# Kernel tuning notes

Measured on AMD Instinct MI355X. Metric: run time of the kernel, lower is better.

The kernel has to match this reference:

```python
import jax, jax.numpy as jnp
import numpy as np

N, E, D_IN, HID, HEADS = 50000, 800000, 128, 32, 8
NEG_SLOPE = 0.2


def gat_conv(x, src, dst, W_src, W_dst, a_src, a_dst, b, heads, ch, concat):
    n = x.shape[0]
    hs = (x @ W_src).reshape(n, heads, ch)  # source-side features [N,H,C]
    hd = (x @ W_dst).reshape(n, heads, ch)  # dest-side features   [N,H,C]
    alpha_s = jnp.einsum('nhc,hc->nh', hs, a_src)  # [N,H]
    alpha_d = jnp.einsum('nhc,hc->nh', hd, a_dst)  # [N,H]
    e = jax.nn.leaky_relu(alpha_s[src] + alpha_d[dst], NEG_SLOPE)  # [E,H]
    # segment softmax over edges grouped by destination node
    m = jax.ops.segment_max(e, dst, num_segments=n)
    m = jnp.where(jnp.isfinite(m), m, 0.0)
    e = jnp.exp(e - jax.lax.stop_gradient(m)[dst])
    denom = jax.ops.segment_sum(e, dst, num_segments=n)
    alpha = e / (denom[dst] + 1e-16)  # [E,H]
    # weighted scatter-aggregate of source features to destinations
    out = jax.ops.segment_sum(hs[src] * alpha[:, :, None], dst, num_segments=n)  # [N,H,C]
    out = out.reshape(n, heads * ch) if concat else out.mean(axis=1)
    return out + b


def setup_inputs() -> dict:
    key = jax.random.key(0)
    ks = jax.random.split(key, 12)
    glorot = lambda k, shape: jax.random.normal(k, shape, jnp.float32) * np.sqrt(2.0 / (shape[0] + shape[-1]))
    x = jax.random.normal(ks[0], (N, D_IN), jnp.float32)
    edge_index = jax.random.randint(ks[1], (2, E), 0, N, jnp.int64)
    return {
        'x': x,
        'edge_index': edge_index,
        'W1_src': glorot(ks[2], (D_IN, HEADS * HID)),
        'W1_dst': glorot(ks[3], (D_IN, HEADS * HID)),
        'a1_src': glorot(ks[4], (HEADS, HID)),
        'a1_dst': glorot(ks[5], (HEADS, HID)),
        'b1': jnp.zeros((HEADS * HID,), jnp.float32),
        'W2_src': glorot(ks[6], (HEADS * HID, HID)),
        'W2_dst': glorot(ks[7], (HEADS * HID, HID)),
        'a2_src': glorot(ks[8], (1, HID)),
        'a2_dst': glorot(ks[9], (1, HID)),
        'b2': jnp.zeros((HID,), jnp.float32),
    }


def reference(x, edge_index, W1_src, W1_dst, a1_src, a1_dst, b1,
              W2_src, W2_dst, a2_src, a2_dst, b2):
    src, dst = edge_index[0], edge_index[1]
    h = gat_conv(x, src, dst, W1_src, W1_dst, a1_src, a1_dst, b1, HEADS, HID, True)
    h = jax.nn.relu(h)
    out = gat_conv(h, src, dst, W2_src, W2_dst, a2_src, a2_dst, b2, 1, HID, True)
    return out
```

## Files before the change

### kernel.cpp

```cpp
#include <hip/hip_runtime.h>
#include <hip/hip_bf16.h>

#define NEG_SLOPE 0.2f

typedef unsigned int uint;
typedef unsigned short ushort;
typedef __attribute__((ext_vector_type(8))) short short8;
typedef __attribute__((ext_vector_type(4))) float floatx4;

static __device__ __forceinline__ ushort f2bf(float f) {
    uint u = __float_as_uint(f);
    uint r = (u + 0x7fffu + ((u >> 16) & 1u)) >> 16;
    return (ushort)r;
}
static __device__ __forceinline__ float bf2f(uint s) {
    return __uint_as_float(s << 16);
}

__global__ __launch_bounds__(256) void convert_x(
    const float* __restrict__ x, ushort* __restrict__ xb, int total4) {
    int i = blockIdx.x * blockDim.x + threadIdx.x;
    if (i >= total4) return;
    float4 v = ((const float4*)x)[i];
    uint2 pk;
    pk.x = (uint)f2bf(v.x) | ((uint)f2bf(v.y) << 16);
    pk.y = (uint)f2bf(v.z) | ((uint)f2bf(v.w) << 16);
    ((uint2*)xb)[i] = pk;
}

__global__ __launch_bounds__(256) void prep_weights(
    const float* __restrict__ W1_src, const float* __restrict__ W2_src,
    const float* __restrict__ W1_dst, const float* __restrict__ a1_dst,
    const float* __restrict__ W2_dst, const float* __restrict__ a2_dst,
    ushort* __restrict__ W1t, ushort* __restrict__ W2t,
    float* __restrict__ wc1, float* __restrict__ wc2) {
    int i = blockIdx.x * blockDim.x + threadIdx.x;
    if (i < 32768) {
        int nc = i & 255, k = i >> 8;
        W1t[nc * 128 + k] = f2bf(W1_src[k * 256 + nc]);
    } else if (i < 32768 + 8192) {
        int i2 = i - 32768;
        int c = i2 & 31, k = i2 >> 5;
        W2t[c * 256 + k] = f2bf(W2_src[k * 32 + c]);
    } else if (i < 32768 + 8192 + 1024) {
        int i3 = i - 32768 - 8192;
        int k = i3 >> 3, h = i3 & 7;
        float s = 0.f;
#pragma unroll
        for (int c = 0; c < 32; ++c)
            s += W1_dst[k * 256 + h * 32 + c] * a1_dst[h * 32 + c];
        wc1[i3] = s;
    } else if (i < 32768 + 8192 + 1024 + 256) {
        int k = i - 32768 - 8192 - 1024;
        float s = 0.f;
#pragma unroll
        for (int c = 0; c < 32; ++c)
            s += W2_dst[k * 32 + c] * a2_dst[c];
        wc2[k] = s;
    }
}

__global__ __launch_bounds__(256) void hist_kernel(
    const int* __restrict__ dst, int* __restrict__ deg, int E) {
    int e = blockIdx.x * blockDim.x + threadIdx.x;
    if (e < E) atomicAdd(&deg[dst[e]], 1);
}

__global__ __launch_bounds__(256) void scan_block(
    const int* __restrict__ deg, int* __restrict__ incl,
    int* __restrict__ bsum, int n) {
    __shared__ int sh[256];
    int tid = threadIdx.x;
    int i = blockIdx.x * 256 + tid;
    sh[tid] = (i < n) ? deg[i] : 0;
    __syncthreads();
    for (int off = 1; off < 256; off <<= 1) {
        int t = (tid >= off) ? sh[tid - off] : 0;
        __syncthreads();
        sh[tid] += t;
        __syncthreads();
    }
    if (i < n) incl[i] = sh[tid];
    if (tid == 255) bsum[blockIdx.x] = sh[255];
}

__global__ __launch_bounds__(256) void scan_top(
    const int* __restrict__ bsum, int* __restrict__ boff, int nb) {
    __shared__ int sh[256];
    int tid = threadIdx.x;
    sh[tid] = (tid < nb) ? bsum[tid] : 0;
    __syncthreads();
    for (int off = 1; off < 256; off <<= 1) {
        int t = (tid >= off) ? sh[tid - off] : 0;
        __syncthreads();
        sh[tid] += t;
        __syncthreads();
    }
    boff[tid] = sh[tid] - ((tid < nb) ? bsum[tid] : 0);
}

__global__ __launch_bounds__(256) void rs_kernel(
    const int* __restrict__ incl, const int* __restrict__ deg,
    const int* __restrict__ boff, int* __restrict__ rs,
    int* __restrict__ cursor, int n) {
    int i = blockIdx.x * blockDim.x + threadIdx.x;
    if (i >= n) return;
    int v = incl[i] - deg[i] + boff[i >> 8];
    rs[i] = v;
    cursor[i] = v;
}

__global__ __launch_bounds__(256) void fill_kernel(
    const int* __restrict__ src, const int* __restrict__ dst,
    int* __restrict__ cursor, int* __restrict__ csr_src, int E) {
    int e = blockIdx.x * blockDim.x + threadIdx.x;
    if (e >= E) return;
    int d = dst[e];
    int pos = atomicAdd(&cursor[d], 1);
    csr_src[pos] = src[e];
}

__global__ __launch_bounds__(256) void gemm1_mfma(
    const ushort* __restrict__ xb, const ushort* __restrict__ W1t,
    const float* __restrict__ a_src, const float* __restrict__ wc1,
    ushort* __restrict__ hs1b, float* __restrict__ as1,
    float* __restrict__ ad1, int n) {
    __shared__ ushort At[128 * 128];
    __shared__ ushort Out[128 * 128];
    int mblk = blockIdx.x >> 1, nhalf = blockIdx.x & 1;
    int m0 = mblk * 128;
    int tid = threadIdx.x;
#pragma unroll
    for (int i = 0; i < 8; ++i) {
        int id = tid + i * 256;
        int m = id >> 4, c = id & 15;
        int gm = m0 + m;
        uint4 v = {0, 0, 0, 0};
        if (gm < n) v = *(const uint4*)(xb + (size_t)gm * 128 + c * 8);
        *(uint4*)(At + m * 128 + ((c ^ (m & 15)) * 8)) = v;
    }
    __syncthreads();
    int wid = tid >> 6, lane = tid & 63;
    int q = lane >> 4, l16 = lane & 15;
    int wm = (wid >> 1) * 64;
    int wn = (wid & 1) * 64;
    int gn0 = nhalf * 128 + wn;
    floatx4 z = {0.f, 0.f, 0.f, 0.f};
    floatx4 acc[4][4];
#pragma unroll
    for (int mt = 0; mt < 4; ++mt)
#pragma unroll
        for (int nt = 0; nt < 4; ++nt) acc[mt][nt] = z;
#pragma unroll
    for (int s = 0; s < 4; ++s) {
        short8 af[4], bf[4];
#pragma unroll
        for (int mt = 0; mt < 4; ++mt) {
            int row = wm + mt * 16 + l16;
            int c = s * 4 + q;
            af[mt] = *(const short8*)(At + row * 128 + ((c ^ (row & 15)) * 8));
        }
#pragma unroll
        for (int nt = 0; nt < 4; ++nt) {
            int col = gn0 + nt * 16 + l16;
            bf[nt] = *(const short8*)(W1t + col * 128 + s * 32 + q * 8);
        }
#pragma unroll
        for (int mt = 0; mt < 4; ++mt)
#pragma unroll
            for (int nt = 0; nt < 4; ++nt)
                acc[mt][nt] = __builtin_amdgcn_mfma_f32_16x16x32_bf16(
                    af[mt], bf[nt], acc[mt][nt], 0, 0, 0);
    }
#pragma unroll
    for (int mt = 0; mt < 4; ++mt)
#pragma unroll
        for (int nt = 0; nt < 4; ++nt) {
            floatx4 a = acc[mt][nt];
            int colL = wn + nt * 16 + l16;
#pragma unroll
            for (int r = 0; r < 4; ++r) {
                int rowL = wm + mt * 16 + q * 4 + r;
                Out[rowL * 128 + colL] = f2bf(a[r]);
            }
        }
    __syncthreads();
#pragma unroll
    for (int i = 0; i < 8; ++i) {
        int id = tid + i * 256;
        int m = id >> 4, c8 = id & 15;
        int gm = m0 + m;
        if (gm < n) {
            uint4 v = *(uint4*)(Out + m * 128 + c8 * 8);
            *(uint4*)(hs1b + (size_t)gm * 256 + nhalf * 128 + c8 * 8) = v;
        }
    }
#pragma unroll
    for (int i = 0; i < 2; ++i) {
        int id = tid + i * 256;
        int m = id & 127, hl = id >> 7;
        int gm = m0 + m;
        if (gm < n) {
            int h = nhalf * 4 + hl;
            const ushort* row = Out + m * 128 + hl * 32;
            const float* av = a_src + h * 32;
            float s = 0.f;
#pragma unroll
            for (int c = 0; c < 32; ++c) s += bf2f(row[c]) * av[c];
            as1[(size_t)gm * 8 + h] = s;
        }
    }
    if (nhalf == 0) {
#pragma unroll
        for (int i = 0; i < 4; ++i) {
            int id = tid + i * 256;
            int m = id & 127, h = id >> 7;
            int gm = m0 + m;
            if (gm < n) {
                float s = 0.f;
                for (int c = 0; c < 16; ++c) {
                    const ushort* p = At + m * 128 + ((c ^ (m & 15)) * 8);
#pragma unroll
                    for (int jj = 0; jj < 8; ++jj)
                        s += bf2f(p[jj]) * wc1[(c * 8 + jj) * 8 + h];
                }
                ad1[(size_t)gm * 8 + h] = s;
            }
        }
    }
}

__global__ __launch_bounds__(256) void gather1(
    const int* __restrict__ csr_src, const int* __restrict__ rs,
    const int* __restrict__ deg, const ushort* __restrict__ hs1b,
    const float* __restrict__ as1, const float* __restrict__ ad1,
    const float* __restrict__ b1, ushort* __restrict__ h1b, int n) {
    int gid = blockIdx.x * blockDim.x + threadIdx.x;
    int node = gid >> 6;
    int lane = threadIdx.x & 63;
    if (node >= n) return;
    int j = lane >> 5, l = lane & 31;
    int h = l >> 2;
    float ad_v = ad1[node * 8 + h];
    int start = rs[node], cnt = deg[node];
    float acc0 = 0.f, acc1 = 0.f, acc2 = 0.f, acc3 = 0.f;
    float acc4 = 0.f, acc5 = 0.f, acc6 = 0.f, acc7 = 0.f;
    float dacc = 0.f;
    int i = j;
    for (; i + 2 < cnt; i += 4) {
        int sA = csr_src[start + i];
        int sB = csr_src[start + i + 2];
        float tA = as1[sA * 8 + h] + ad_v;
        float tB = as1[sB * 8 + h] + ad_v;
        uint4 vA = *(const uint4*)(hs1b + (size_t)sA * 256 + l * 8);
        uint4 vB = *(const uint4*)(hs1b + (size_t)sB * 256 + l * 8);
        tA = (tA >= 0.f) ? tA : NEG_SLOPE * tA;
        tB = (tB >= 0.f) ? tB : NEG_SLOPE * tB;
        float wA = __expf(tA);
        float wB = __expf(tB);
        acc0 += bf2f(vA.x & 0xffffu) * wA + bf2f(vB.x & 0xffffu) * wB;
        acc1 += bf2f(vA.x >> 16) * wA + bf2f(vB.x >> 16) * wB;
        acc2 += bf2f(vA.y & 0xffffu) * wA + bf2f(vB.y & 0xffffu) * wB;
        acc3 += bf2f(vA.y >> 16) * wA + bf2f(vB.y >> 16) * wB;
        acc4 += bf2f(vA.z & 0xffffu) * wA + bf2f(vB.z & 0xffffu) * wB;
        acc5 += bf2f(vA.z >> 16) * wA + bf2f(vB.z >> 16) * wB;
        acc6 += bf2f(vA.w & 0xffffu) * wA + bf2f(vB.w & 0xffffu) * wB;
        acc7 += bf2f(vA.w >> 16) * wA + bf2f(vB.w >> 16) * wB;
        dacc += wA + wB;
    }
    for (; i < cnt; i += 2) {
        int s = csr_src[start + i];
        float t = as1[s * 8 + h] + ad_v;
        uint4 v = *(const uint4*)(hs1b + (size_t)s * 256 + l * 8);
        t = (t >= 0.f) ? t : NEG_SLOPE * t;
        float w = __expf(t);
        acc0 += bf2f(v.x & 0xffffu) * w;
        acc1 += bf2f(v.x >> 16) * w;
        acc2 += bf2f(v.y & 0xffffu) * w;
        acc3 += bf2f(v.y >> 16) * w;
        acc4 += bf2f(v.z & 0xffffu) * w;
        acc5 += bf2f(v.z >> 16) * w;
        acc6 += bf2f(v.w & 0xffffu) * w;
        acc7 += bf2f(v.w >> 16) * w;
        dacc += w;
    }
    acc0 += __shfl_xor(acc0, 32, 64);
    acc1 += __shfl_xor(acc1, 32, 64);
    acc2 += __shfl_xor(acc2, 32, 64);
    acc3 += __shfl_xor(acc3, 32, 64);
    acc4 += __shfl_xor(acc4, 32, 64);
    acc5 += __shfl_xor(acc5, 32, 64);
    acc6 += __shfl_xor(acc6, 32, 64);
    acc7 += __shfl_xor(acc7, 32, 64);
    dacc += __shfl_xor(dacc, 32, 64);
    if (j == 0) {
        float inv = 1.f / (dacc + 1e-16f);
        float4 b0 = ((const float4*)b1)[l * 2];
        float4 b4 = ((const float4*)b1)[l * 2 + 1];
        float o0 = fmaxf(fmaf(acc0, inv, b0.x), 0.f);
        float o1 = fmaxf(fmaf(acc1, inv, b0.y), 0.f);
        float o2 = fmaxf(fmaf(acc2, inv, b0.z), 0.f);
        float o3 = fmaxf(fmaf(acc3, inv, b0.w), 0.f);
        float o4 = fmaxf(fmaf(acc4, inv, b4.x), 0.f);
        float o5 = fmaxf(fmaf(acc5, inv, b4.y), 0.f);
        float o6 = fmaxf(fmaf(acc6, inv, b4.z), 0.f);
        float o7 = fmaxf(fmaf(acc7, inv, b4.w), 0.f);
        uint4 pk;
        pk.x = (uint)f2bf(o0) | ((uint)f2bf(o1) << 16);
        pk.y = (uint)f2bf(o2) | ((uint)f2bf(o3) << 16);
        pk.z = (uint)f2bf(o4) | ((uint)f2bf(o5) << 16);
        pk.w = (uint)f2bf(o6) | ((uint)f2bf(o7) << 16);
        *(uint4*)(h1b + (size_t)node * 256 + l * 8) = pk;
    }
}

__global__ __launch_bounds__(256) void gemm2_mfma(
    const ushort* __restrict__ h1b, const ushort* __restrict__ W2t,
    const float* __restrict__ a2_src, const float* __restrict__ wc2,
    ushort* __restrict__ hs2b, float* __restrict__ as2,
    float* __restrict__ ad2, int n) {
    __shared__ ushort At[128 * 256];
    __shared__ ushort Out[128 * 32];
    int m0 = blockIdx.x * 128;
    int tid = threadIdx.x;
#pragma unroll
    for (int i = 0; i < 16; ++i) {
        int id = tid + i * 256;
        int m = id >> 5, c = id & 31;
        int gm = m0 + m;
        uint4 v = {0, 0, 0, 0};
        if (gm < n) v = *(const uint4*)(h1b + (size_t)gm * 256 + c * 8);
        *(uint4*)(At + m * 256 + ((c ^ (m & 15)) * 8)) = v;
    }
    __syncthreads();
    int wid = tid >> 6, lane = tid & 63;
    int q = lane >> 4, l16 = lane & 15;
    int wm = wid * 32;
    floatx4 z = {0.f, 0.f, 0.f, 0.f};
    floatx4 acc[2][2] = {{z, z}, {z, z}};
#pragma unroll
    for (int s = 0; s < 8; ++s) {
        short8 af[2], bf[2];
#pragma unroll
        for (int mt = 0; mt < 2; ++mt) {
            int row = wm + mt * 16 + l16;
            int c = s * 4 + q;
            af[mt] = *(const short8*)(At + row * 256 + ((c ^ (row & 15)) * 8));
        }
#pragma unroll
        for (int nt = 0; nt < 2; ++nt) {
            int col = nt * 16 + l16;
            bf[nt] = *(const short8*)(W2t + col * 256 + s * 32 + q * 8);
        }
#pragma unroll
        for (int mt = 0; mt < 2; ++mt)
#pragma unroll
            for (int nt = 0; nt < 2; ++nt)
                acc[mt][nt] = __builtin_amdgcn_mfma_f32_16x16x32_bf16(
                    af[mt], bf[nt], acc[mt][nt], 0, 0, 0);
    }
#pragma unroll
    for (int mt = 0; mt < 2; ++mt)
#pragma unroll
        for (int nt = 0; nt < 2; ++nt) {
            floatx4 a = acc[mt][nt];
            int colL = nt * 16 + l16;
#pragma unroll
            for (int r = 0; r < 4; ++r) {
                int rowL = wm + mt * 16 + q * 4 + r;
                Out[rowL * 32 + colL] = f2bf(a[r]);
            }
        }
    __syncthreads();
#pragma unroll
    for (int i = 0; i < 2; ++i) {
        int id = tid + i * 256;
        int c4 = id & 3, m = id >> 2;
        int gm = m0 + m;
        if (gm < n)
            *(uint4*)(hs2b + (size_t)gm * 32 + c4 * 8) =
                *(uint4*)(Out + m * 32 + c4 * 8);
    }
    if (tid < 128) {
        int gm = m0 + tid;
        if (gm < n) {
            float s = 0.f;
#pragma unroll
            for (int c2 = 0; c2 < 32; ++c2)
                s += bf2f(Out[tid * 32 + c2]) * a2_src[c2];
            as2[gm] = s;
        }
    } else {
        int m = tid - 128, gm = m0 + m;
        if (gm < n) {
            float s = 0.f;
            for (int c = 0; c < 32; ++c) {
                const ushort* p = At + m * 256 + ((c ^ (m & 15)) * 8);
#pragma unroll
                for (int jj = 0; jj < 8; ++jj)
                    s += bf2f(p[jj]) * wc2[c * 8 + jj];
            }
            ad2[gm] = s;
        }
    }
}

__global__ __launch_bounds__(256) void gather2(
    const int* __restrict__ csr_src, const int* __restrict__ rs,
    const int* __restrict__ deg, const ushort* __restrict__ hs2b,
    const float* __restrict__ as2, const float* __restrict__ ad2,
    const float* __restrict__ b2, float* __restrict__ out, int n) {
    int gid = blockIdx.x * blockDim.x + threadIdx.x;
    int node = gid >> 6;
    int lane = threadIdx.x & 63;
    if (node >= n) return;
    int j = lane >> 4, l = lane & 15;
    float ad_v = ad2[node];
    int start = rs[node], cnt = deg[node];
    float accx = 0.f, accy = 0.f, dacc = 0.f;
    for (int i = j; i < cnt; i += 4) {
        int s = csr_src[start + i];
        float t = as2[s] + ad_v;
        t = (t >= 0.f) ? t : NEG_SLOPE * t;
        float w = __expf(t);
        uint v = *(const uint*)(hs2b + (size_t)s * 32 + l * 2);
        accx += bf2f(v & 0xffffu) * w;
        accy += bf2f(v >> 16) * w;
        dacc += w;
    }
    accx += __shfl_xor(accx, 32, 64);
    accy += __shfl_xor(accy, 32, 64);
    dacc += __shfl_xor(dacc, 32, 64);
    accx += __shfl_xor(accx, 16, 64);
    accy += __shfl_xor(accy, 16, 64);
    dacc += __shfl_xor(dacc, 16, 64);
    if (lane < 16) {
        float inv = 1.f / (dacc + 1e-16f);
        float2 bv = ((const float2*)b2)[l];
        float2 o;
        o.x = fmaf(accx, inv, bv.x);
        o.y = fmaf(accy, inv, bv.y);
        *(float2*)(out + (size_t)node * 32 + l * 2) = o;
    }
}

extern "C" void kernel_launch(void* const* d_in, const int* in_sizes, int n_in,
                              void* d_out, int out_size, void* d_ws, size_t ws_size,
                              hipStream_t stream) {
    const float* x      = (const float*)d_in[0];
    const int*   eidx   = (const int*)d_in[1];
    const float* W1_src = (const float*)d_in[2];
    const float* W1_dst = (const float*)d_in[3];
    const float* a1_src = (const float*)d_in[4];
    const float* a1_dst = (const float*)d_in[5];
    const float* b1     = (const float*)d_in[6];
    const float* W2_src = (const float*)d_in[7];
    const float* W2_dst = (const float*)d_in[8];
    const float* a2_src = (const float*)d_in[9];
    const float* a2_dst = (const float*)d_in[10];
    const float* b2     = (const float*)d_in[11];

    const int n = in_sizes[0] / 128;
    const int E = in_sizes[1] / 2;
    const int* src = eidx;
    const int* dst = eidx + E;
    const int nb = (n + 255) / 256;

    char* ws = (char*)d_ws;
    size_t o = 0;
    auto alloc = [&](size_t bytes) {
        void* p = ws + o;
        o += (bytes + 255) & ~(size_t)255;
        return p;
    };
    ushort* xb   = (ushort*)alloc((size_t)n * 128 * 2);
    ushort* W1t  = (ushort*)alloc(256 * 128 * 2);
    ushort* W2t  = (ushort*)alloc(32 * 256 * 2);
    ushort* hs1b = (ushort*)alloc((size_t)n * 256 * 2);
    ushort* h1b  = (ushort*)alloc((size_t)n * 256 * 2);
    ushort* hs2b = (ushort*)alloc((size_t)n * 32 * 2);
    float* as1 = (float*)alloc((size_t)n * 8 * 4);
    float* ad1 = (float*)alloc((size_t)n * 8 * 4);
    float* as2 = (float*)alloc((size_t)n * 4);
    float* ad2 = (float*)alloc((size_t)n * 4);
    float* wc1 = (float*)alloc(1024 * 4);
    float* wc2 = (float*)alloc(256 * 4);
    int* deg     = (int*)alloc((size_t)n * 4);
    int* incl    = (int*)alloc((size_t)n * 4);
    int* bsum    = (int*)alloc(256 * 4);
    int* boff    = (int*)alloc(256 * 4);
    int* rs      = (int*)alloc((size_t)n * 4);
    int* cursor  = (int*)alloc((size_t)n * 4);
    int* csr_src = (int*)alloc((size_t)E * 4);

    hipMemsetAsync(deg, 0, (size_t)n * sizeof(int), stream);

    hist_kernel<<<(E + 255) / 256, 256, 0, stream>>>(dst, deg, E);
    scan_block<<<nb, 256, 0, stream>>>(deg, incl, bsum, n);
    scan_top<<<1, 256, 0, stream>>>(bsum, boff, nb);
    rs_kernel<<<nb, 256, 0, stream>>>(incl, deg, boff, rs, cursor, n);
    fill_kernel<<<(E + 255) / 256, 256, 0, stream>>>(src, dst, cursor, csr_src, E);

    convert_x<<<(n * 32 + 255) / 256, 256, 0, stream>>>(x, xb, n * 32);
    prep_weights<<<(32768 + 8192 + 1024 + 256 + 255) / 256, 256, 0, stream>>>(
        W1_src, W2_src, W1_dst, a1_dst, W2_dst, a2_dst, W1t, W2t, wc1, wc2);

    gemm1_mfma<<<((n + 127) / 128) * 2, 256, 0, stream>>>(
        xb, W1t, a1_src, wc1, hs1b, as1, ad1, n);
    gather1<<<(n + 3) / 4, 256, 0, stream>>>(
        csr_src, rs, deg, hs1b, as1, ad1, b1, h1b, n);

    gemm2_mfma<<<(n + 127) / 128, 256, 0, stream>>>(
        h1b, W2t, a2_src, wc2, hs2b, as2, ad2, n);
    gather2<<<(n + 3) / 4, 256, 0, stream>>>(
        csr_src, rs, deg, hs2b, as2, ad2, b2, (float*)d_out, n);
}
```

Baseline: 341.8 us.

## Fuse bf16 conversion into gemm1, merge scan kernels, widen gather2 edge parallelism

Drops the separate convert_x pass: gemm1 now reads fp32 x and converts it to bf16 while staging tiles in LDS, which removes a full write and reread of x. The scan_top kernel is folded into rs_kernel, where each block recomputes the block-offset scan itself, and rs gets an n+1 sentinel so the gathers no longer read deg. gather2 now processes 8 edges per wavefront, each lane handling 4 channels, trading a longer shuffle reduction for more edge-level parallelism. Since gemm1 runs two column-half blocks per row tile, x is read and converted twice.

```diff
diff --git a/kernel.cpp b/kernel.cpp
--- a/kernel.cpp
+++ b/kernel.cpp
@@ -17,15 +17,63 @@
     return __uint_as_float(s << 16);
 }
 
-__global__ __launch_bounds__(256) void convert_x(
-    const float* __restrict__ x, ushort* __restrict__ xb, int total4) {
-    int i = blockIdx.x * blockDim.x + threadIdx.x;
-    if (i >= total4) return;
-    float4 v = ((const float4*)x)[i];
-    uint2 pk;
-    pk.x = (uint)f2bf(v.x) | ((uint)f2bf(v.y) << 16);
-    pk.y = (uint)f2bf(v.z) | ((uint)f2bf(v.w) << 16);
-    ((uint2*)xb)[i] = pk;
+__global__ __launch_bounds__(256) void hist_kernel(
+    const int* __restrict__ dst, int* __restrict__ deg, int E) {
+    int e = blockIdx.x * blockDim.x + threadIdx.x;
+    if (e < E) atomicAdd(&deg[dst[e]], 1);
+}
+
+__global__ __launch_bounds__(256) void scan_block(
+    const int* __restrict__ deg, int* __restrict__ rs,
+    int* __restrict__ bsum, int n) {
+    __shared__ int sh[256];
+    int tid = threadIdx.x;
+    int i = blockIdx.x * 256 + tid;
+    sh[tid] = (i < n) ? deg[i] : 0;
+    __syncthreads();
+    for (int off = 1; off < 256; off <<= 1) {
+        int t = (tid >= off) ? sh[tid - off] : 0;
+        __syncthreads();
+        sh[tid] += t;
+        __syncthreads();
+    }
+    if (i < n) rs[i] = sh[tid];
+    if (tid == 255) bsum[blockIdx.x] = sh[255];
+}
+
+__global__ __launch_bounds__(256) void rs_kernel(
+    const int* __restrict__ deg, const int* __restrict__ bsum,
+    int* __restrict__ rs, int* __restrict__ cursor, int n, int E, int nb) {
+    __shared__ int sh[256];
+    int tid = threadIdx.x;
+    int own = (tid < nb) ? bsum[tid] : 0;
+    sh[tid] = own;
+    __syncthreads();
+    for (int off = 1; off < 256; off <<= 1) {
+        int t = (tid >= off) ? sh[tid - off] : 0;
+        __syncthreads();
+        sh[tid] += t;
+        __syncthreads();
+    }
+    int boff = sh[blockIdx.x] - ((blockIdx.x < nb) ? bsum[blockIdx.x] : 0);
+    __syncthreads();
+    int i = blockIdx.x * 256 + tid;
+    if (i < n) {
+        int v = rs[i] - deg[i] + boff;
+        rs[i] = v;
+        cursor[i] = v;
+    }
+    if (i == 0) rs[n] = E;
+}
+
+__global__ __launch_bounds__(256) void fill_kernel(
+    const int* __restrict__ src, const int* __restrict__ dst,
+    int* __restrict__ cursor, int* __restrict__ csr_src, int E) {
+    int e = blockIdx.x * blockDim.x + threadIdx.x;
+    if (e >= E) return;
+    int d = dst[e];
+    int pos = atomicAdd(&cursor[d], 1);
+    csr_src[pos] = src[e];
 }
 
 __global__ __launch_bounds__(256) void prep_weights(
@@ -60,68 +108,8 @@
     }
 }
 
-__global__ __launch_bounds__(256) void hist_kernel(
-    const int* __restrict__ dst, int* __restrict__ deg, int E) {
-    int e = blockIdx.x * blockDim.x + threadIdx.x;
-    if (e < E) atomicAdd(&deg[dst[e]], 1);
-}
-
-__global__ __launch_bounds__(256) void scan_block(
-    const int* __restrict__ deg, int* __restrict__ incl,
-    int* __restrict__ bsum, int n) {
-    __shared__ int sh[256];
-    int tid = threadIdx.x;
-    int i = blockIdx.x * 256 + tid;
-    sh[tid] = (i < n) ? deg[i] : 0;
-    __syncthreads();
-    for (int off = 1; off < 256; off <<= 1) {
-        int t = (tid >= off) ? sh[tid - off] : 0;
-        __syncthreads();
-        sh[tid] += t;
-        __syncthreads();
-    }
-    if (i < n) incl[i] = sh[tid];
-    if (tid == 255) bsum[blockIdx.x] = sh[255];
-}
-
-__global__ __launch_bounds__(256) void scan_top(
-    const int* __restrict__ bsum, int* __restrict__ boff, int nb) {
-    __shared__ int sh[256];
-    int tid = threadIdx.x;
-    sh[tid] = (tid < nb) ? bsum[tid] : 0;
-    __syncthreads();
-    for (int off = 1; off < 256; off <<= 1) {
-        int t = (tid >= off) ? sh[tid - off] : 0;
-        __syncthreads();
-        sh[tid] += t;
-        __syncthreads();
-    }
-    boff[tid] = sh[tid] - ((tid < nb) ? bsum[tid] : 0);
-}
-
-__global__ __launch_bounds__(256) void rs_kernel(
-    const int* __restrict__ incl, const int* __restrict__ deg,
-    const int* __restrict__ boff, int* __restrict__ rs,
-    int* __restrict__ cursor, int n) {
-    int i = blockIdx.x * blockDim.x + threadIdx.x;
-    if (i >= n) return;
-    int v = incl[i] - deg[i] + boff[i >> 8];
-    rs[i] = v;
-    cursor[i] = v;
-}
-
-__global__ __launch_bounds__(256) void fill_kernel(
-    const int* __restrict__ src, const int* __restrict__ dst,
-    int* __restrict__ cursor, int* __restrict__ csr_src, int E) {
-    int e = blockIdx.x * blockDim.x + threadIdx.x;
-    if (e >= E) return;
-    int d = dst[e];
-    int pos = atomicAdd(&cursor[d], 1);
-    csr_src[pos] = src[e];
-}
-
 __global__ __launch_bounds__(256) void gemm1_mfma(
-    const ushort* __restrict__ xb, const ushort* __restrict__ W1t,
+    const float* __restrict__ x, const ushort* __restrict__ W1t,
     const float* __restrict__ a_src, const float* __restrict__ wc1,
     ushort* __restrict__ hs1b, float* __restrict__ as1,
     float* __restrict__ ad1, int n) {
@@ -135,9 +123,16 @@
         int id = tid + i * 256;
         int m = id >> 4, c = id & 15;
         int gm = m0 + m;
-        uint4 v = {0, 0, 0, 0};
-        if (gm < n) v = *(const uint4*)(xb + (size_t)gm * 128 + c * 8);
-        *(uint4*)(At + m * 128 + ((c ^ (m & 15)) * 8)) = v;
+        uint4 pk = {0, 0, 0, 0};
+        if (gm < n) {
+            const float4* xp = (const float4*)(x + (size_t)gm * 128 + c * 8);
+            float4 v0 = xp[0], v1 = xp[1];
+            pk.x = (uint)f2bf(v0.x) | ((uint)f2bf(v0.y) << 16);
+            pk.y = (uint)f2bf(v0.z) | ((uint)f2bf(v0.w) << 16);
+            pk.z = (uint)f2bf(v1.x) | ((uint)f2bf(v1.y) << 16);
+            pk.w = (uint)f2bf(v1.z) | ((uint)f2bf(v1.w) << 16);
+        }
+        *(uint4*)(At + m * 128 + ((c ^ (m & 15)) * 8)) = pk;
     }
     __syncthreads();
     int wid = tid >> 6, lane = tid & 63;
@@ -232,9 +227,9 @@
 
 __global__ __launch_bounds__(256) void gather1(
     const int* __restrict__ csr_src, const int* __restrict__ rs,
-    const int* __restrict__ deg, const ushort* __restrict__ hs1b,
-    const float* __restrict__ as1, const float* __restrict__ ad1,
-    const float* __restrict__ b1, ushort* __restrict__ h1b, int n) {
+    const ushort* __restrict__ hs1b, const float* __restrict__ as1,
+    const float* __restrict__ ad1, const float* __restrict__ b1,
+    ushort* __restrict__ h1b, int n) {
     int gid = blockIdx.x * blockDim.x + threadIdx.x;
     int node = gid >> 6;
     int lane = threadIdx.x & 63;
@@ -242,7 +237,7 @@
     int j = lane >> 5, l = lane & 31;
     int h = l >> 2;
     float ad_v = ad1[node * 8 + h];
-    int start = rs[node], cnt = deg[node];
+    int start = rs[node], cnt = rs[node + 1] - start;
     float acc0 = 0.f, acc1 = 0.f, acc2 = 0.f, acc3 = 0.f;
     float acc4 = 0.f, acc5 = 0.f, acc6 = 0.f, acc7 = 0.f;
     float dacc = 0.f;
@@ -407,40 +402,46 @@
 
 __global__ __launch_bounds__(256) void gather2(
     const int* __restrict__ csr_src, const int* __restrict__ rs,
-    const int* __restrict__ deg, const ushort* __restrict__ hs2b,
-    const float* __restrict__ as2, const float* __restrict__ ad2,
-    const float* __restrict__ b2, float* __restrict__ out, int n) {
+    const ushort* __restrict__ hs2b, const float* __restrict__ as2,
+    const float* __restrict__ ad2, const float* __restrict__ b2,
+    float* __restrict__ out, int n) {
     int gid = blockIdx.x * blockDim.x + threadIdx.x;
     int node = gid >> 6;
     int lane = threadIdx.x & 63;
     if (node >= n) return;
-    int j = lane >> 4, l = lane & 15;
+    int g = lane >> 3, l = lane & 7;
     float ad_v = ad2[node];
-    int start = rs[node], cnt = deg[node];
-    float accx = 0.f, accy = 0.f, dacc = 0.f;
-    for (int i = j; i < cnt; i += 4) {
+    int start = rs[node], cnt = rs[node + 1] - start;
+    float a0 = 0.f, a1 = 0.f, a2 = 0.f, a3 = 0.f, dacc = 0.f;
+    for (int i = g; i < cnt; i += 8) {
         int s = csr_src[start + i];
         float t = as2[s] + ad_v;
         t = (t >= 0.f) ? t : NEG_SLOPE * t;
         float w = __expf(t);
-        uint v = *(const uint*)(hs2b + (size_t)s * 32 + l * 2);
-        accx += bf2f(v & 0xffffu) * w;
-        accy += bf2f(v >> 16) * w;
+        uint2 v = *(const uint2*)(hs2b + (size_t)s * 32 + l * 4);
+        a0 += bf2f(v.x & 0xffffu) * w;
+        a1 += bf2f(v.x >> 16) * w;
+        a2 += bf2f(v.y & 0xffffu) * w;
+        a3 += bf2f(v.y >> 16) * w;
         dacc += w;
     }
-    accx += __shfl_xor(accx, 32, 64);
-    accy += __shfl_xor(accy, 32, 64);
-    dacc += __shfl_xor(dacc, 32, 64);
-    accx += __shfl_xor(accx, 16, 64);
-    accy += __shfl_xor(accy, 16, 64);
-    dacc += __shfl_xor(dacc, 16, 64);
-    if (lane < 16) {
+#pragma unroll
+    for (int m = 8; m <= 32; m <<= 1) {
+        a0 += __shfl_xor(a0, m, 64);
+        a1 += __shfl_xor(a1, m, 64);
+        a2 += __shfl_xor(a2, m, 64);
+        a3 += __shfl_xor(a3, m, 64);
+        dacc += __shfl_xor(dacc, m, 64);
+    }
+    if (g == 0) {
         float inv = 1.f / (dacc + 1e-16f);
-        float2 bv = ((const float2*)b2)[l];
-        float2 o;
-        o.x = fmaf(accx, inv, bv.x);
-        o.y = fmaf(accy, inv, bv.y);
-        *(float2*)(out + (size_t)node * 32 + l * 2) = o;
+        float4 bv = ((const float4*)b2)[l];
+        float4 o;
+        o.x = fmaf(a0, inv, bv.x);
+        o.y = fmaf(a1, inv, bv.y);
+        o.z = fmaf(a2, inv, bv.z);
+        o.w = fmaf(a3, inv, bv.w);
+        *(float4*)(out + (size_t)node * 32 + l * 4) = o;
     }
 }
 
@@ -462,8 +463,8 @@
 
     const int n = in_sizes[0] / 128;
     const int E = in_sizes[1] / 2;
-    const int* src = eidx;
-    const int* dst = eidx + E;
+    const int* srcp = eidx;
+    const int* dstp = eidx + E;
     const int nb = (n + 255) / 256;
 
     char* ws = (char*)d_ws;
@@ -473,7 +474,6 @@
         o += (bytes + 255) & ~(size_t)255;
         return p;
     };
-    ushort* xb   = (ushort*)alloc((size_t)n * 128 * 2);
     ushort* W1t  = (ushort*)alloc(256 * 128 * 2);
     ushort* W2t  = (ushort*)alloc(32 * 256 * 2);
     ushort* hs1b = (ushort*)alloc((size_t)n * 256 * 2);
@@ -486,32 +486,29 @@
     float* wc1 = (float*)alloc(1024 * 4);
     float* wc2 = (float*)alloc(256 * 4);
     int* deg     = (int*)alloc((size_t)n * 4);
-    int* incl    = (int*)alloc((size_t)n * 4);
+    int* rs      = (int*)alloc(((size_t)n + 1) * 4);
+    int* cursor  = (int*)alloc((size_t)n * 4);
     int* bsum    = (int*)alloc(256 * 4);
-    int* boff    = (int*)alloc(256 * 4);
-    int* rs      = (int*)alloc((size_t)n * 4);
-    int* cursor  = (int*)alloc((size_t)n * 4);
     int* csr_src = (int*)alloc((size_t)E * 4);
 
     hipMemsetAsync(deg, 0, (size_t)n * sizeof(int), stream);
 
-    hist_kernel<<<(E + 255) / 256, 256, 0, stream>>>(dst, deg, E);
-    scan_block<<<nb, 256, 0, stream>>>(deg, incl, bsum, n);
-    scan_top<<<1, 256, 0, stream>>>(bsum, boff, nb);
-    rs_kernel<<<nb, 256, 0, stream>>>(incl, deg, boff, rs, cursor, n);
-    fill_kernel<<<(E + 255) / 256, 256, 0, stream>>>(src, dst, cursor, csr_src, E);
-
-    convert_x<<<(n * 32 + 255) / 256, 256, 0, stream>>>(x, xb, n * 32);
+    hist_kernel<<<(E + 255) / 256, 256, 0, stream>>>(dstp, deg, E);
+    scan_block<<<nb, 256, 0, stream>>>(deg, rs, bsum, n);
+    rs_kernel<<<nb, 256, 0, stream>>>(deg, bsum, rs, cursor, n, E, nb);
+    fill_kernel<<<(E + 255) / 256, 256, 0, stream>>>(srcp, dstp, cursor,
+                                                     csr_src, E);
+
     prep_weights<<<(32768 + 8192 + 1024 + 256 + 255) / 256, 256, 0, stream>>>(
         W1_src, W2_src, W1_dst, a1_dst, W2_dst, a2_dst, W1t, W2t, wc1, wc2);
 
     gemm1_mfma<<<((n + 127) / 128) * 2, 256, 0, stream>>>(
-        xb, W1t, a1_src, wc1, hs1b, as1, ad1, n);
+        x, W1t, a1_src, wc1, hs1b, as1, ad1, n);
     gather1<<<(n + 3) / 4, 256, 0, stream>>>(
-        csr_src, rs, deg, hs1b, as1, ad1, b1, h1b, n);
+        csr_src, rs, hs1b, as1, ad1, b1, h1b, n);
 
     gemm2_mfma<<<(n + 127) / 128, 256, 0, stream>>>(
         h1b, W2t, a2_src, wc2, hs2b, as2, ad2, n);
     gather2<<<(n + 3) / 4, 256, 0, stream>>>(
-        csr_src, rs, deg, hs2b, as2, ad2, b2, (float*)d_out, n);
-}
+        csr_src, rs, hs2b, as2, ad2, b2, (float*)d_out, n);
+}
```

Measured after the change: 326.4 us. 1.05x faster.
